# Kernel optimization log

Measured on AMD Instinct MI355X. Metric: run time of the kernel, lower is better.

## Reference

```python
import jax, jax.numpy as jnp
import numpy as np

TABLE_SZ = 2 ** 14
FEAT_DIM = 2
NUM_LEVELS = 16
MIN_RES = 16.0
MAX_RES = 512.0
B = 1 << 20

# corner order v0..v7 from get_nearest_vertices_coords (z-ascending, ccw)
OFFSETS = jnp.array([[0, 0, 0], [1, 0, 0], [1, 1, 0], [0, 1, 0],
                     [0, 0, 1], [1, 0, 1], [1, 1, 1], [0, 1, 1]], dtype=jnp.int32)


def setup_inputs() -> dict:
    key = jax.random.key(0)
    kx, kt = jax.random.split(key)
    x = jax.random.uniform(kx, (B, 3), dtype=jnp.float32)  # coords in [0,1)
    # RandomUniform(-1e-4, 1e-4) initializer for all 16 tables, stacked
    tables = jax.random.uniform(kt, (NUM_LEVELS, TABLE_SZ, FEAT_DIM),
                                dtype=jnp.float32, minval=-1e-4, maxval=1e-4)
    return {"x": x, "tables": tables}


def reference(x, tables):
    # per-level resolutions: floor(min_res * b**l), b geometric growth factor
    b = jnp.exp((jnp.log(MAX_RES) - jnp.log(MIN_RES)) / (NUM_LEVELS - 1))
    res = jnp.floor(MIN_RES * b ** jnp.arange(NUM_LEVELS, dtype=jnp.float32))  # [L]

    # NOTE: original computes interp weights from the UNSCALED position
    # (position - floor(position)); since x in [0,1) this equals x. Faithful.
    w = x - jnp.floor(x)  # [B,3]
    off = OFFSETS.astype(bool)[None]  # [1,8,3]
    # trilinear weight per corner: prod over xyz of (w if offset else 1-w)
    cw = jnp.prod(jnp.where(off, w[:, None, :], 1.0 - w[:, None, :]), axis=-1)  # [B,8]

    P1 = jnp.uint32(2654435761)
    P2 = jnp.uint32(805459861)
    TS = jnp.uint32(TABLE_SZ)

    def level(carry, lvl):
        table, r = lvl  # [T,F], scalar
        sp = r * x  # [B,3]
        low = jnp.floor(sp).astype(jnp.int32)
        high = jnp.ceil(sp).astype(jnp.int32)
        corners = jnp.where(off, high[:, None, :], low[:, None, :]).astype(jnp.uint32)  # [B,8,3]
        # spatial hash: x ^ (p1*y) ^ (p2*z) mod table_sz (uint32 wraparound;
        # table_sz is a power of two so this matches int32-wrap + floormod)
        h = (corners[..., 0] ^ (P1 * corners[..., 1]) ^ (P2 * corners[..., 2])) % TS
        feats = table[h.astype(jnp.int32)]  # gather -> [B,8,F]
        return carry, jnp.einsum('bkf,bk->bf', feats, cw)  # [B,F]

    _, outs = jax.lax.scan(level, None, (tables, res))  # [L,B,F]
    # matches tf.concat over levels along feature axis
    return jnp.transpose(outs, (1, 0, 2)).reshape(x.shape[0], NUM_LEVELS * FEAT_DIM)
```

## Files before the change

### kernel.cpp

```cpp
#include <hip/hip_runtime.h>
#include <cmath>

#define TABLE_SZ 16384
#define NLEV 16

struct ResArr { float r[NLEV]; };

__global__ __launch_bounds__(256) void cvt_tables(
    const float* __restrict__ src, uint32_t* __restrict__ dst, int n_entries)
{
    int i = blockIdx.x * blockDim.x + threadIdx.x;
    int e = i * 4;
    if (e + 3 < n_entries) {
        const float4* s4 = (const float4*)(src) + i * 2;
        float4 a = s4[0], b = s4[1];
        float v[8] = {a.x,a.y,a.z,a.w,b.x,b.y,b.z,b.w};
        uint32_t o[4];
        #pragma unroll
        for (int k = 0; k < 4; ++k) {
            unsigned short lo = __builtin_bit_cast(unsigned short, (_Float16)v[2*k+0]);
            unsigned short hi = __builtin_bit_cast(unsigned short, (_Float16)v[2*k+1]);
            o[k] = (uint32_t)lo | ((uint32_t)hi << 16);
        }
        *(uint4*)(dst + e) = make_uint4(o[0], o[1], o[2], o[3]);
    }
}

template <int TBLOCK>
__device__ __forceinline__ void stage_h(const uint32_t* __restrict__ tb, int l,
                                        uint32_t* buf, int tid, int wid)
{
    const char* gbase = (const char*)tb + (size_t)l * (TABLE_SZ * 4);
    #pragma unroll
    for (int j = 0; j < (TABLE_SZ * 4) / (TBLOCK * 16); ++j) {
        uint32_t goff = (uint32_t)(j * (TBLOCK * 16) + tid * 16);
        uint32_t loff = (uint32_t)(j * (TBLOCK * 16) + wid * 1024);
        __builtin_amdgcn_global_load_lds(
            (const __attribute__((address_space(1))) uint32_t*)(gbase + goff),
            (__attribute__((address_space(3))) uint32_t*)((char*)buf + loff),
            16, 0, 0);
    }
}

__device__ __forceinline__ float2 level_accum_h(const uint32_t* tab, float r,
                                                float px, float py, float pz,
                                                const float* cw)
{
    const uint32_t P1 = 2654435761u, P2 = 805459861u;
    const uint32_t m  = TABLE_SZ - 1u;

    float sx = r*px, sy = r*py, sz = r*pz;
    uint32_t lx = (uint32_t)sx,  hx = (uint32_t)ceilf(sx);
    uint32_t ly = (uint32_t)sy,  hy = (uint32_t)ceilf(sy);
    uint32_t lz = (uint32_t)sz,  hz = (uint32_t)ceilf(sz);
    uint32_t yl = P1*ly;
    uint32_t yh = (hy == ly) ? yl : yl + P1;
    uint32_t zl = P2*lz;
    uint32_t zh = (hz == lz) ? zl : zl + P2;

    uint32_t h0 = (lx ^ yl ^ zl) & m;
    uint32_t h1 = (hx ^ yl ^ zl) & m;
    uint32_t h2 = (hx ^ yh ^ zl) & m;
    uint32_t h3 = (lx ^ yh ^ zl) & m;
    uint32_t h4 = (lx ^ yl ^ zh) & m;
    uint32_t h5 = (hx ^ yl ^ zh) & m;
    uint32_t h6 = (hx ^ yh ^ zh) & m;
    uint32_t h7 = (lx ^ yh ^ zh) & m;

    uint32_t v0 = tab[h0], v1 = tab[h1], v2 = tab[h2], v3 = tab[h3];
    uint32_t v4 = tab[h4], v5 = tab[h5], v6 = tab[h6], v7 = tab[h7];

    float a0 = 0.f, a1 = 0.f;
    uint32_t vv[8] = {v0,v1,v2,v3,v4,v5,v6,v7};
    #pragma unroll
    for (int k = 0; k < 8; ++k) {
        _Float16 lo = __builtin_bit_cast(_Float16, (unsigned short)(vv[k] & 0xFFFFu));
        _Float16 hi = __builtin_bit_cast(_Float16, (unsigned short)(vv[k] >> 16));
        a0 += (float)lo * cw[k];
        a1 += (float)hi * cw[k];
    }
    return make_float2(a0, a1);
}

template <int TBLOCK, int TPPT>
__global__ __launch_bounds__(TBLOCK) void mrhe_db(
    const float* __restrict__ x,
    const uint32_t* __restrict__ tb,
    float* __restrict__ out,
    ResArr res, int B)
{
    constexpr int ROUNDS = (TABLE_SZ * 4) / (TBLOCK * 16);
    static_assert(ROUNDS == 8 || ROUNDS == 16, "vmcnt literal must match");

    __shared__ uint32_t tab[2][TABLE_SZ];

    const int tid  = threadIdx.x;
    const int wid  = tid >> 6;
    const int base = blockIdx.x * (TBLOCK * TPPT);

    float px[TPPT], py[TPPT], pz[TPPT];
    float cw[TPPT][8];
    #pragma unroll
    for (int p = 0; p < TPPT; ++p) {
        int idx = base + p * TBLOCK + tid;
        size_t j = (idx < B) ? (size_t)idx : 0;
        px[p] = x[3*j+0]; py[p] = x[3*j+1]; pz[p] = x[3*j+2];
        float ax = 1.0f - px[p], ay = 1.0f - py[p], az = 1.0f - pz[p];
        cw[p][0] = (ax*ay)*az;          cw[p][1] = (px[p]*ay)*az;
        cw[p][2] = (px[p]*py[p])*az;    cw[p][3] = (ax*py[p])*az;
        cw[p][4] = (ax*ay)*pz[p];       cw[p][5] = (px[p]*ay)*pz[p];
        cw[p][6] = (px[p]*py[p])*pz[p]; cw[p][7] = (ax*py[p])*pz[p];
    }

    stage_h<TBLOCK>(tb, 0, tab[0], tid, wid);

    float o[TPPT][16];

    #pragma unroll
    for (int l = 0; l < NLEV; ++l) {
        if (l + 1 < NLEV) {
            stage_h<TBLOCK>(tb, l + 1, tab[(l + 1) & 1], tid, wid);
            if constexpr (ROUNDS == 8)
                asm volatile("s_waitcnt vmcnt(8)" ::: "memory");
            else
                asm volatile("s_waitcnt vmcnt(16)" ::: "memory");
        } else {
            asm volatile("s_waitcnt vmcnt(0)" ::: "memory");
        }
        asm volatile("s_barrier" ::: "memory");

        const uint32_t* buf = tab[l & 1];
        #pragma unroll
        for (int p = 0; p < TPPT; ++p) {
            float2 a = level_accum_h(buf, res.r[l], px[p], py[p], pz[p], cw[p]);
            o[p][2*(l & 7) + 0] = a.x;
            o[p][2*(l & 7) + 1] = a.y;
        }

        if ((l & 7) == 7) {
            const int half = l >> 3;
            #pragma unroll
            for (int p = 0; p < TPPT; ++p) {
                int idx = base + p * TBLOCK + tid;
                if (idx < B) {
                    float* po = out + (size_t)idx * (2*NLEV) + half * 16;
                    #pragma unroll
                    for (int q = 0; q < 4; ++q) {
                        float4 v;
                        v.x = o[p][4*q+0]; v.y = o[p][4*q+1];
                        v.z = o[p][4*q+2]; v.w = o[p][4*q+3];
                        ((float4*)po)[q] = v;
                    }
                }
            }
        }

        asm volatile("s_barrier" ::: "memory");
    }
}

__global__ __launch_bounds__(256) void mrhe_direct(
    const float* __restrict__ x,
    const float* __restrict__ tables,
    float* __restrict__ out,
    ResArr res, int B)
{
    int i = blockIdx.x * blockDim.x + threadIdx.x;
    if (i >= B) return;
    float px = x[3*(size_t)i+0], py = x[3*(size_t)i+1], pz = x[3*(size_t)i+2];
    float ax = 1.0f - px, ay = 1.0f - py, az = 1.0f - pz;
    float cw[8] = {(ax*ay)*az,(px*ay)*az,(px*py)*az,(ax*py)*az,
                   (ax*ay)*pz,(px*ay)*pz,(px*py)*pz,(ax*py)*pz};
    const uint32_t P1 = 2654435761u, P2 = 805459861u, m = TABLE_SZ - 1u;
    float o[2*NLEV];
    #pragma unroll
    for (int l = 0; l < NLEV; ++l) {
        float r = res.r[l];
        float sx = r*px, sy = r*py, sz = r*pz;
        uint32_t lx = (uint32_t)sx, hx = (uint32_t)ceilf(sx);
        uint32_t ly = (uint32_t)sy, hy = (uint32_t)ceilf(sy);
        uint32_t lz = (uint32_t)sz, hz = (uint32_t)ceilf(sz);
        uint32_t yl = P1*ly, yh = P1*hy, zl = P2*lz, zh = P2*hz;
        uint32_t h[8] = {(lx^yl^zl)&m,(hx^yl^zl)&m,(hx^yh^zl)&m,(lx^yh^zl)&m,
                         (lx^yl^zh)&m,(hx^yl^zh)&m,(hx^yh^zh)&m,(lx^yh^zh)&m};
        const float2* tbl = (const float2*)tables + (size_t)l * TABLE_SZ;
        float a0 = 0.f, a1 = 0.f;
        #pragma unroll
        for (int k = 0; k < 8; ++k) {
            float2 f = tbl[h[k]];
            a0 += f.x * cw[k]; a1 += f.y * cw[k];
        }
        o[2*l+0] = a0; o[2*l+1] = a1;
    }
    float4* po = (float4*)(out + (size_t)i * (2*NLEV));
    #pragma unroll
    for (int q = 0; q < (2*NLEV)/4; ++q) {
        float4 v; v.x = o[4*q+0]; v.y = o[4*q+1]; v.z = o[4*q+2]; v.w = o[4*q+3];
        po[q] = v;
    }
}

extern "C" void kernel_launch(void* const* d_in, const int* in_sizes, int n_in,
                              void* d_out, int out_size, void* d_ws, size_t ws_size,
                              hipStream_t stream)
{
    const float* x      = (const float*)d_in[0];
    const float* tables = (const float*)d_in[1];
    float* out = (float*)d_out;
    int B = in_sizes[0] / 3;

    ResArr res;
    float bgrow = expf((logf(512.0f) - logf(16.0f)) / 15.0f);
    for (int l = 0; l < NLEV; ++l)
        res.r[l] = floorf(16.0f * powf(bgrow, (float)l));

    const int n_entries = NLEV * TABLE_SZ;
    const size_t need = (size_t)n_entries * 4;

    if (ws_size >= need && d_ws) {
        uint32_t* tb = (uint32_t*)d_ws;
        hipLaunchKernelGGL(cvt_tables, dim3(n_entries/4/256), dim3(256), 0, stream,
                           tables, tb, n_entries);

        hipFuncAttributes attr{};
        hipError_t e = hipFuncGetAttributes(&attr, (const void*)mrhe_db<512, 2>);
        bool use512 = (e == hipSuccess) && (attr.localSizeBytes == 0);

        if (use512) {
            int per_block = 512 * 2;
            int grid = (B + per_block - 1) / per_block;
            hipLaunchKernelGGL((mrhe_db<512, 2>), dim3(grid), dim3(512), 0, stream,
                               x, tb, out, res, B);
        } else {
            int per_block = 256 * 4;
            int grid = (B + per_block - 1) / per_block;
            hipLaunchKernelGGL((mrhe_db<256, 4>), dim3(grid), dim3(256), 0, stream,
                               x, tb, out, res, B);
        }
    } else {
        int grid = (B + 255) / 256;
        hipLaunchKernelGGL(mrhe_direct, dim3(grid), dim3(256), 0, stream,
                           x, tables, out, res, B);
    }
}
```

Before: 109.2 us.

## Serve two levels via direct global gathers overlapped with LDS staging

Adds a new kernel that stages only 14 of the 16 level tables into LDS (double-buffered). Levels 13 and 15 are fetched straight from the fp32 global tables with inline-asm dwordx2 gathers, issued a few levels early so their latency overlaps the LDS work. The goal is to cut the per-block LDS staging traffic and the number of barrier rounds. In exchange it adds scattered global gathers, a hand-tuned vmcnt accounting that must stay matched to the staging load count, and extra registers to hold the in-flight results.

```diff
diff --git a/kernel.cpp b/kernel.cpp
--- a/kernel.cpp
+++ b/kernel.cpp
@@ -3,6 +3,10 @@
 
 #define TABLE_SZ 16384
 #define NLEV 16
+#define BLOCK 512
+#define PPT 2
+
+typedef float v2f __attribute__((ext_vector_type(2)));
 
 struct ResArr { float r[NLEV]; };
 
@@ -42,13 +46,11 @@
     }
 }
 
-__device__ __forceinline__ float2 level_accum_h(const uint32_t* tab, float r,
-                                                float px, float py, float pz,
-                                                const float* cw)
+struct C8 { uint32_t h[8]; };
+__device__ __forceinline__ C8 corner_idx(float r, float px, float py, float pz)
 {
     const uint32_t P1 = 2654435761u, P2 = 805459861u;
     const uint32_t m  = TABLE_SZ - 1u;
-
     float sx = r*px, sy = r*py, sz = r*pz;
     uint32_t lx = (uint32_t)sx,  hx = (uint32_t)ceilf(sx);
     uint32_t ly = (uint32_t)sy,  hy = (uint32_t)ceilf(sy);
@@ -57,21 +59,27 @@
     uint32_t yh = (hy == ly) ? yl : yl + P1;
     uint32_t zl = P2*lz;
     uint32_t zh = (hz == lz) ? zl : zl + P2;
-
-    uint32_t h0 = (lx ^ yl ^ zl) & m;
-    uint32_t h1 = (hx ^ yl ^ zl) & m;
-    uint32_t h2 = (hx ^ yh ^ zl) & m;
-    uint32_t h3 = (lx ^ yh ^ zl) & m;
-    uint32_t h4 = (lx ^ yl ^ zh) & m;
-    uint32_t h5 = (hx ^ yl ^ zh) & m;
-    uint32_t h6 = (hx ^ yh ^ zh) & m;
-    uint32_t h7 = (lx ^ yh ^ zh) & m;
-
-    uint32_t v0 = tab[h0], v1 = tab[h1], v2 = tab[h2], v3 = tab[h3];
-    uint32_t v4 = tab[h4], v5 = tab[h5], v6 = tab[h6], v7 = tab[h7];
-
+    C8 c;
+    c.h[0] = (lx ^ yl ^ zl) & m;
+    c.h[1] = (hx ^ yl ^ zl) & m;
+    c.h[2] = (hx ^ yh ^ zl) & m;
+    c.h[3] = (lx ^ yh ^ zl) & m;
+    c.h[4] = (lx ^ yl ^ zh) & m;
+    c.h[5] = (hx ^ yl ^ zh) & m;
+    c.h[6] = (hx ^ yh ^ zh) & m;
+    c.h[7] = (lx ^ yh ^ zh) & m;
+    return c;
+}
+
+__device__ __forceinline__ float2 level_accum_h(const uint32_t* tab, float r,
+                                                float px, float py, float pz,
+                                                const float* cw)
+{
+    C8 c = corner_idx(r, px, py, pz);
+    uint32_t vv[8];
+    #pragma unroll
+    for (int k = 0; k < 8; ++k) vv[k] = tab[c.h[k]];
     float a0 = 0.f, a1 = 0.f;
-    uint32_t vv[8] = {v0,v1,v2,v3,v4,v5,v6,v7};
     #pragma unroll
     for (int k = 0; k < 8; ++k) {
         _Float16 lo = __builtin_bit_cast(_Float16, (unsigned short)(vv[k] & 0xFFFFu));
@@ -80,6 +88,158 @@
         a1 += (float)hi * cw[k];
     }
     return make_float2(a0, a1);
+}
+
+__device__ __forceinline__ void ta_issue(const v2f* __restrict__ t, float r,
+                                         float px, float py, float pz, v2f* g)
+{
+    C8 c = corner_idx(r, px, py, pz);
+    #pragma unroll
+    for (int kk = 0; kk < 8; ++kk) {
+        const v2f* p = t + c.h[kk];
+        asm volatile("global_load_dwordx2 %0, %1, off"
+                     : "=&v"(g[kk]) : "v"(p) : "memory");
+    }
+}
+
+__global__ __launch_bounds__(BLOCK) void mrhe_ta(
+    const float* __restrict__ x,
+    const v2f* __restrict__ ftab,
+    const uint32_t* __restrict__ tb,
+    float* __restrict__ out,
+    ResArr res, int B)
+{
+    __shared__ uint32_t tab[2][TABLE_SZ];
+
+    const int tid  = threadIdx.x;
+    const int wid  = tid >> 6;
+    const int base = blockIdx.x * (BLOCK * PPT);
+
+    float px[PPT], py[PPT], pz[PPT];
+    float cw[PPT][8];
+    #pragma unroll
+    for (int p = 0; p < PPT; ++p) {
+        int idx = base + p * BLOCK + tid;
+        size_t j = (idx < B) ? (size_t)idx : 0;
+        px[p] = x[3*j+0]; py[p] = x[3*j+1]; pz[p] = x[3*j+2];
+        float ax = 1.0f - px[p], ay = 1.0f - py[p], az = 1.0f - pz[p];
+        cw[p][0] = (ax*ay)*az;          cw[p][1] = (px[p]*ay)*az;
+        cw[p][2] = (px[p]*py[p])*az;    cw[p][3] = (ax*py[p])*az;
+        cw[p][4] = (ax*ay)*pz[p];       cw[p][5] = (px[p]*ay)*pz[p];
+        cw[p][6] = (px[p]*py[p])*pz[p]; cw[p][7] = (ax*py[p])*pz[p];
+    }
+
+    asm volatile("" ::: "memory");
+    stage_h<BLOCK>(tb, 0, tab[0], tid, wid);
+    asm volatile("" ::: "memory");
+
+    float o[PPT][16];
+    v2f g13[PPT][8], g15[PPT][8];
+
+    #pragma unroll
+    for (int k = 0; k < 14; ++k) {
+        const int lev = (k < 13) ? k : 14;
+
+        if (k < 13) {
+            const int nl = (k + 1 < 13) ? (k + 1) : 14;
+            asm volatile("" ::: "memory");
+            stage_h<BLOCK>(tb, nl, tab[(k + 1) & 1], tid, wid);
+            asm volatile("" ::: "memory");
+        }
+
+        if (k == 9 || k == 12)
+            asm volatile("s_waitcnt vmcnt(24)" ::: "memory");
+        else if (k == 13)
+            asm volatile("s_waitcnt vmcnt(0)" ::: "memory");
+        else
+            asm volatile("s_waitcnt vmcnt(8)" ::: "memory");
+        __builtin_amdgcn_sched_barrier(0);
+        asm volatile("s_barrier" ::: "memory");
+
+        if (k == 11) {
+            #pragma unroll
+            for (int p = 0; p < PPT; ++p) {
+                float b0 = 0.f, b1 = 0.f;
+                #pragma unroll
+                for (int kk = 0; kk < 8; ++kk) {
+                    asm volatile("" : "+v"(g13[p][kk]));
+                    b0 += g13[p][kk].x * cw[p][kk];
+                    b1 += g13[p][kk].y * cw[p][kk];
+                }
+                o[p][10] = b0; o[p][11] = b1;
+            }
+        }
+        if (k == 13) {
+            #pragma unroll
+            for (int p = 0; p < PPT; ++p) {
+                float b0 = 0.f, b1 = 0.f;
+                #pragma unroll
+                for (int kk = 0; kk < 8; ++kk) {
+                    asm volatile("" : "+v"(g15[p][kk]));
+                    b0 += g15[p][kk].x * cw[p][kk];
+                    b1 += g15[p][kk].y * cw[p][kk];
+                }
+                o[p][14] = b0; o[p][15] = b1;
+            }
+        }
+
+        {
+            const uint32_t* buf = tab[k & 1];
+            #pragma unroll
+            for (int p = 0; p < PPT; ++p) {
+                float2 a = level_accum_h(buf, res.r[lev], px[p], py[p], pz[p], cw[p]);
+                o[p][2*(lev & 7) + 0] = a.x;
+                o[p][2*(lev & 7) + 1] = a.y;
+            }
+        }
+
+        if (k == 7) {
+            #pragma unroll
+            for (int p = 0; p < PPT; ++p) {
+                int idx = base + p * BLOCK + tid;
+                if (idx < B) {
+                    float* po = out + (size_t)idx * (2*NLEV);
+                    #pragma unroll
+                    for (int q = 0; q < 4; ++q) {
+                        float4 v;
+                        v.x = o[p][4*q+0]; v.y = o[p][4*q+1];
+                        v.z = o[p][4*q+2]; v.w = o[p][4*q+3];
+                        ((float4*)po)[q] = v;
+                    }
+                }
+            }
+        }
+
+        if (k == 8) {
+            #pragma unroll
+            for (int p = 0; p < PPT; ++p)
+                ta_issue(ftab + (size_t)13 * TABLE_SZ, res.r[13],
+                         px[p], py[p], pz[p], g13[p]);
+        }
+        if (k == 11) {
+            #pragma unroll
+            for (int p = 0; p < PPT; ++p)
+                ta_issue(ftab + (size_t)15 * TABLE_SZ, res.r[15],
+                         px[p], py[p], pz[p], g15[p]);
+        }
+
+        asm volatile("s_barrier" ::: "memory");
+    }
+
+    #pragma unroll
+    for (int p = 0; p < PPT; ++p) {
+        int idx = base + p * BLOCK + tid;
+        if (idx < B) {
+            float* po = out + (size_t)idx * (2*NLEV) + 16;
+            #pragma unroll
+            for (int q = 0; q < 4; ++q) {
+                float4 v;
+                v.x = o[p][4*q+0]; v.y = o[p][4*q+1];
+                v.z = o[p][4*q+2]; v.w = o[p][4*q+3];
+                ((float4*)po)[q] = v;
+            }
+        }
+    }
 }
 
 template <int TBLOCK, int TPPT>
@@ -89,9 +249,6 @@
     float* __restrict__ out,
     ResArr res, int B)
 {
-    constexpr int ROUNDS = (TABLE_SZ * 4) / (TBLOCK * 16);
-    static_assert(ROUNDS == 8 || ROUNDS == 16, "vmcnt literal must match");
-
     __shared__ uint32_t tab[2][TABLE_SZ];
 
     const int tid  = threadIdx.x;
@@ -120,10 +277,7 @@
     for (int l = 0; l < NLEV; ++l) {
         if (l + 1 < NLEV) {
             stage_h<TBLOCK>(tb, l + 1, tab[(l + 1) & 1], tid, wid);
-            if constexpr (ROUNDS == 8)
-                asm volatile("s_waitcnt vmcnt(8)" ::: "memory");
-            else
-                asm volatile("s_waitcnt vmcnt(16)" ::: "memory");
+            asm volatile("s_waitcnt vmcnt(8)" ::: "memory");
         } else {
             asm volatile("s_waitcnt vmcnt(0)" ::: "memory");
         }
@@ -171,23 +325,15 @@
     float ax = 1.0f - px, ay = 1.0f - py, az = 1.0f - pz;
     float cw[8] = {(ax*ay)*az,(px*ay)*az,(px*py)*az,(ax*py)*az,
                    (ax*ay)*pz,(px*ay)*pz,(px*py)*pz,(ax*py)*pz};
-    const uint32_t P1 = 2654435761u, P2 = 805459861u, m = TABLE_SZ - 1u;
     float o[2*NLEV];
     #pragma unroll
     for (int l = 0; l < NLEV; ++l) {
-        float r = res.r[l];
-        float sx = r*px, sy = r*py, sz = r*pz;
-        uint32_t lx = (uint32_t)sx, hx = (uint32_t)ceilf(sx);
-        uint32_t ly = (uint32_t)sy, hy = (uint32_t)ceilf(sy);
-        uint32_t lz = (uint32_t)sz, hz = (uint32_t)ceilf(sz);
-        uint32_t yl = P1*ly, yh = P1*hy, zl = P2*lz, zh = P2*hz;
-        uint32_t h[8] = {(lx^yl^zl)&m,(hx^yl^zl)&m,(hx^yh^zl)&m,(lx^yh^zl)&m,
-                         (lx^yl^zh)&m,(hx^yl^zh)&m,(hx^yh^zh)&m,(lx^yh^zh)&m};
+        C8 c = corner_idx(res.r[l], px, py, pz);
         const float2* tbl = (const float2*)tables + (size_t)l * TABLE_SZ;
         float a0 = 0.f, a1 = 0.f;
         #pragma unroll
         for (int k = 0; k < 8; ++k) {
-            float2 f = tbl[h[k]];
+            float2 f = tbl[c.h[k]];
             a0 += f.x * cw[k]; a1 += f.y * cw[k];
         }
         o[2*l+0] = a0; o[2*l+1] = a1;
@@ -223,19 +369,19 @@
                            tables, tb, n_entries);
 
         hipFuncAttributes attr{};
-        hipError_t e = hipFuncGetAttributes(&attr, (const void*)mrhe_db<512, 2>);
-        bool use512 = (e == hipSuccess) && (attr.localSizeBytes == 0);
-
-        if (use512) {
+        hipError_t e = hipFuncGetAttributes(&attr, (const void*)mrhe_ta);
+        bool useTa = (e == hipSuccess) && (attr.localSizeBytes == 0);
+
+        if (useTa) {
+            int per_block = BLOCK * PPT;
+            int grid = (B + per_block - 1) / per_block;
+            hipLaunchKernelGGL(mrhe_ta, dim3(grid), dim3(BLOCK), 0, stream,
+                               x, (const v2f*)tables, tb, out, res, B);
+        } else {
             int per_block = 512 * 2;
             int grid = (B + per_block - 1) / per_block;
             hipLaunchKernelGGL((mrhe_db<512, 2>), dim3(grid), dim3(512), 0, stream,
                                x, tb, out, res, B);
-        } else {
-            int per_block = 256 * 4;
-            int grid = (B + per_block - 1) / per_block;
-            hipLaunchKernelGGL((mrhe_db<256, 4>), dim3(grid), dim3(256), 0, stream,
-                               x, tb, out, res, B);
         }
     } else {
         int grid = (B + 255) / 256;
```

After: 134.8 us. 1.23x slower.
